# Kernel tuning notes

Measured on AMD Instinct MI355X. Metric: run time of the kernel, lower is better.

Reference implementation:

```python
import jax, jax.numpy as jnp
import numpy as np

B, H, S, D = 4, 16, 2048, 64


def setup_inputs() -> dict:
    key = jax.random.key(0)
    kq, kk, kv = jax.random.split(key, 3)
    Q = jax.random.normal(kq, (B, H, S, D), dtype=jnp.float32)
    K = jax.random.normal(kk, (B, H, S, D), dtype=jnp.float32)
    V = jax.random.normal(kv, (B, H, S, D), dtype=jnp.float32)
    mask = jnp.ones((1, 1, S, S), dtype=jnp.int32)
    return {"Q": Q, "K": K, "V": V, "mask": mask}


def reference(Q, K, V, mask):
    d_k = Q.shape[-1]
    scale = 1.0 / jnp.sqrt(jnp.asarray(d_k, dtype=Q.dtype))
    # [B, H, S, S] attention scores
    attn = jnp.einsum('bhqd,bhkd->bhqk', Q, K) * scale
    # mask == 0 -> -1e9 (matches torch boolean-index assignment)
    attn = jnp.where(mask == 0, jnp.asarray(-1e9, dtype=attn.dtype), attn)
    softmax_attn = jax.nn.softmax(attn, axis=-1)
    out = jnp.einsum('bhqk,bhkd->bhqd', softmax_attn, V)
    return out
```

## Files before the change

### kernel.cpp

```cpp
#include <hip/hip_runtime.h>

typedef __bf16 bf16;
typedef __attribute__((ext_vector_type(8))) __bf16 bf16x8;
typedef __attribute__((ext_vector_type(8))) ushort ushort8v;
typedef __attribute__((ext_vector_type(4))) ushort ushort4v;
typedef __attribute__((ext_vector_type(16))) float f32x16;

constexpr int S_LEN = 2048;
constexpr int DH    = 64;
constexpr int QBLK  = 128;
constexpr int KVBLK = 64;
constexpr int NWAVE = 4;
constexpr int NT    = S_LEN / KVBLK;
constexpr float QSCALE = 0.125f * 1.44269504088896f;
constexpr float NEG    = -1.44269504e9f;
constexpr float THR    = 8.0f;
constexpr size_t TILE_BYTES = (size_t)KVBLK * DH * 2;
constexpr size_t KV_BYTES   = (size_t)64 * NT * TILE_BYTES;

__device__ __forceinline__ ushort bfb(float f) {
  bf16 b = (bf16)f;
  return __builtin_bit_cast(ushort, b);
}
__device__ __forceinline__ int SWZ(int row) {
  return ((row & 7) ^ ((row >> 3) & 7)) << 4;
}
__device__ __forceinline__ uint cvtpk(float lo, float hi) {
  uint r;
  asm("v_cvt_pk_bf16_f32 %0, %1, %2" : "=v"(r) : "v"(lo), "v"(hi));
  return r;
}
__device__ __forceinline__ void gload16(const char* g, void* l) {
  __builtin_amdgcn_global_load_lds(
      (__attribute__((address_space(1))) void*)(g),
      (__attribute__((address_space(3))) void*)(l), 16, 0, 0);
}

__global__ __launch_bounds__(256)
void cvt_kv(const float* __restrict__ K, const float* __restrict__ V,
            const int* __restrict__ M, char* __restrict__ kws,
            char* __restrict__ vws, uint* __restrict__ F) {
  const int t = blockIdx.x, bh = blockIdx.y, tid = threadIdx.x;
  const float* Kb = K + ((size_t)bh * S_LEN + t * KVBLK) * DH;
  const float* Vb = V + ((size_t)bh * S_LEN + t * KVBLK) * DH;
  char* kd = kws + ((size_t)bh * NT + t) * TILE_BYTES;
  char* vd = vws + ((size_t)bh * NT + t) * TILE_BYTES;

  const int kr0 = tid >> 3, kc8 = tid & 7;
#pragma unroll
  for (int h = 0; h < 2; ++h) {
    const int row = kr0 + 32 * h;
    const float* kp = Kb + (size_t)row * DH + kc8 * 8;
    float4 a = *(const float4*)kp;
    float4 b = *(const float4*)(kp + 4);
    ushort8v pk;
    pk[0]=bfb(a.x); pk[1]=bfb(a.y); pk[2]=bfb(a.z); pk[3]=bfb(a.w);
    pk[4]=bfb(b.x); pk[5]=bfb(b.y); pk[6]=bfb(b.z); pk[7]=bfb(b.w);
    *(ushort8v*)(kd + row * 128 + ((kc8 * 16) ^ SWZ(row))) = pk;
  }
  const int vr = (tid >> 4) * 4, vc = (tid & 15) * 4;
  float rr[4][4];
#pragma unroll
  for (int i = 0; i < 4; ++i)
    *(float4*)rr[i] = *(const float4*)(Vb + (size_t)(vr + i) * DH + vc);
#pragma unroll
  for (int c = 0; c < 4; ++c) {
    const int d = vc + c;
    ushort4v p4;
    p4[0]=bfb(rr[0][c]); p4[1]=bfb(rr[1][c]);
    p4[2]=bfb(rr[2][c]); p4[3]=bfb(rr[3][c]);
    *(ushort4v*)(vd + d * 128 + ((vr * 2) ^ SWZ(d))) = p4;
  }

  if (bh < 8) {
    const int qt = t, g = bh;
    const int r  = tid >> 2;
    const int c0 = (tid & 3) * 16;
    __shared__ int s[4];
    uint bits = 0;
    for (int i = 0; i < 4; ++i) {
      const int kt = g * 4 + i;
      const int* row = M + (size_t)(qt * 64 + r) * S_LEN + kt * 64 + c0;
      int ok = 1;
#pragma unroll
      for (int j = 0; j < 4; ++j) {
        int4 v = *(const int4*)(row + j * 4);
        ok &= (v.x != 0) & (v.y != 0) & (v.z != 0) & (v.w != 0);
      }
      ok = __all(ok) ? 1 : 0;
      if ((tid & 63) == 0) s[tid >> 6] = ok;
      __syncthreads();
      if (s[0] & s[1] & s[2] & s[3]) bits |= 1u << kt;
      __syncthreads();
    }
    if (tid == 0) F[qt * 8 + g] = bits;
  }
}

template<bool PRE>
__global__ __launch_bounds__(256, 4)
void attn_fwd(const float* __restrict__ Q, const float* __restrict__ K,
              const float* __restrict__ V, const int* __restrict__ M,
              const uint* __restrict__ F, const char* __restrict__ kws,
              const char* __restrict__ vws, float* __restrict__ O)
{
  __shared__ __align__(16) ushort kb[KVBLK * DH];
  __shared__ __align__(16) ushort vb[KVBLK * DH];

  const int tid  = threadIdx.x;
  const int lane = tid & 63;
  const int w    = tid >> 6;
  const int ql   = lane & 31;
  const int h    = lane >> 5;

  const int flat = blockIdx.y * gridDim.x + blockIdx.x;
  const int nid  = (flat & 7) * 128 + (flat >> 3);
  const int q0   = (nid & 15) * QBLK;
  const int bh   = nid >> 4;

  const float* Qb = Q + ((size_t)bh * S_LEN) * DH;
  const float* Kb = K + ((size_t)bh * S_LEN) * DH;
  const float* Vb = V + ((size_t)bh * S_LEN) * DH;

  uint fmask = 0u;
  if (PRE) {
    uint fm0 = 0u, fm1 = 0u;
#pragma unroll
    for (int g = 0; g < 8; ++g) {
      fm0 |= F[(q0 >> 6) * 8 + g];
      fm1 |= F[((q0 >> 6) + 1) * 8 + g];
    }
    fmask = fm0 & fm1;
  }

  bf16x8 qf[4];
  {
    const float* qp = Qb + (size_t)(q0 + w * 32 + ql) * DH + 8 * h;
#pragma unroll
    for (int s = 0; s < 4; ++s) {
      float4 a = *(const float4*)(qp + 16 * s);
      float4 b = *(const float4*)(qp + 16 * s + 4);
      bf16x8 t2;
      t2[0]=(bf16)(a.x*QSCALE); t2[1]=(bf16)(a.y*QSCALE);
      t2[2]=(bf16)(a.z*QSCALE); t2[3]=(bf16)(a.w*QSCALE);
      t2[4]=(bf16)(b.x*QSCALE); t2[5]=(bf16)(b.y*QSCALE);
      t2[6]=(bf16)(b.z*QSCALE); t2[7]=(bf16)(b.w*QSCALE);
      qf[s] = t2;
    }
  }

  f32x16 acc0, acc1;
#pragma unroll
  for (int i = 0; i < 16; ++i) { acc0[i] = 0.f; acc1[i] = 0.f; }
  float mrow = -1e30f;
  float rsum = 0.f;

  int kofs[2][4];
#pragma unroll
  for (int x = 0; x < 2; ++x) {
    const int row = 32 * x + ql;
    const int sw  = SWZ(row);
#pragma unroll
    for (int s = 0; s < 4; ++s)
      kofs[x][s] = row * 128 + ((32 * s + 16 * h) ^ sw);
  }

  auto mkfrag = [&](float p0, float p1, float p2, float p3,
                    float p4, float p5, float p6, float p7) -> bf16x8 {
    uint a0 = cvtpk(p0, p1), a1 = cvtpk(p2, p3);
    uint b0 = cvtpk(p4, p5), b1 = cvtpk(p6, p7);
    uint ta0 = __shfl_xor(a0, 32), ta1 = __shfl_xor(a1, 32);
    uint tb0 = __shfl_xor(b0, 32), tb1 = __shfl_xor(b1, 32);
    uint4 wv;
    wv.x = h ? tb0 : a0;
    wv.y = h ? tb1 : a1;
    wv.z = h ? b0  : ta0;
    wv.w = h ? b1  : ta1;
    return __builtin_bit_cast(bf16x8, wv);
  };

  const int kr0 = tid >> 3, kc8 = tid & 7;
  const int vr = (tid >> 4) * 4, vc = (tid & 15) * 4;

  for (int t = 0; t < NT; ++t) {
    if (PRE) {
      const char* ksrc = kws + ((size_t)bh * NT + t) * TILE_BYTES;
      const char* vsrc = vws + ((size_t)bh * NT + t) * TILE_BYTES;
#pragma unroll
      for (int c = 0; c < 2; ++c) {
        const int off = (w + c * 4) * 1024 + lane * 16;
        gload16(ksrc + off, (char*)kb + off);
        gload16(vsrc + off, (char*)vb + off);
      }
    } else {
#pragma unroll
      for (int hh = 0; hh < 2; ++hh) {
        const int row = kr0 + 32 * hh;
        const float* kp = Kb + (size_t)(t * KVBLK + row) * DH + kc8 * 8;
        float4 a = *(const float4*)kp;
        float4 b = *(const float4*)(kp + 4);
        ushort8v pk;
        pk[0]=bfb(a.x); pk[1]=bfb(a.y); pk[2]=bfb(a.z); pk[3]=bfb(a.w);
        pk[4]=bfb(b.x); pk[5]=bfb(b.y); pk[6]=bfb(b.z); pk[7]=bfb(b.w);
        *(ushort8v*)((char*)kb + row * 128 + ((kc8 * 16) ^ SWZ(row))) = pk;
      }
      float rr[4][4];
#pragma unroll
      for (int i = 0; i < 4; ++i)
        *(float4*)rr[i] = *(const float4*)(Vb + (size_t)(t * KVBLK + vr + i) * DH + vc);
#pragma unroll
      for (int c = 0; c < 4; ++c) {
        const int d = vc + c;
        ushort4v p4;
        p4[0]=bfb(rr[0][c]); p4[1]=bfb(rr[1][c]);
        p4[2]=bfb(rr[2][c]); p4[3]=bfb(rr[3][c]);
        *(ushort4v*)((char*)vb + d * 128 + ((vr * 2) ^ SWZ(d))) = p4;
      }
    }
    __syncthreads();

    f32x16 sc0, sc1;
#pragma unroll
    for (int i = 0; i < 16; ++i) { sc0[i] = 0.f; sc1[i] = 0.f; }

    __builtin_amdgcn_s_setprio(1);
#pragma unroll
    for (int s = 0; s < 4; ++s) {
      bf16x8 k0 = *(const bf16x8*)((const char*)kb + kofs[0][s]);
      bf16x8 k1 = *(const bf16x8*)((const char*)kb + kofs[1][s]);
      sc0 = __builtin_amdgcn_mfma_f32_32x32x16_bf16(k0, qf[s], sc0, 0,0,0);
      sc1 = __builtin_amdgcn_mfma_f32_32x32x16_bf16(k1, qf[s], sc1, 0,0,0);
    }
    __builtin_amdgcn_s_setprio(0);

    const bool allset = PRE ? (((fmask >> t) & 1u) != 0u) : false;
    if (!allset) {
      const size_t mo = (size_t)(q0 + w * 32 + ql) * S_LEN + t * KVBLK + 4 * h;
#pragma unroll
      for (int r = 0; r < 16; ++r) {
        const int cr = (r & 3) + 8 * (r >> 2);
        if (M[mo + cr] == 0)      sc0[r] = NEG;
        if (M[mo + 32 + cr] == 0) sc1[r] = NEG;
      }
    }

    float lm = fmaxf(sc0[0], sc0[1]);
#pragma unroll
    for (int i = 2; i < 16; ++i) lm = fmaxf(lm, sc0[i]);
#pragma unroll
    for (int i = 0; i < 16; ++i) lm = fmaxf(lm, sc1[i]);
    lm = fmaxf(lm, __shfl_xor(lm, 32));

    if (!__all(lm - mrow <= THR)) {
      const float mnew = fmaxf(mrow, lm);
      const float corr = __builtin_amdgcn_exp2f(mrow - mnew);
      rsum *= corr;
      acc0 *= corr;
      acc1 *= corr;
      mrow = mnew;
    }

    float ps = 0.f;
#pragma unroll
    for (int i = 0; i < 16; ++i) {
      sc0[i] = __builtin_amdgcn_exp2f(sc0[i] - mrow); ps += sc0[i];
      sc1[i] = __builtin_amdgcn_exp2f(sc1[i] - mrow); ps += sc1[i];
    }
    rsum += ps;

    bf16x8 pf[4];
    pf[0] = mkfrag(sc0[0], sc0[1], sc0[2],  sc0[3],  sc0[4],  sc0[5],  sc0[6],  sc0[7]);
    pf[1] = mkfrag(sc0[8], sc0[9], sc0[10], sc0[11], sc0[12], sc0[13], sc0[14], sc0[15]);
    pf[2] = mkfrag(sc1[0], sc1[1], sc1[2],  sc1[3],  sc1[4],  sc1[5],  sc1[6],  sc1[7]);
    pf[3] = mkfrag(sc1[8], sc1[9], sc1[10], sc1[11], sc1[12], sc1[13], sc1[14], sc1[15]);

    __builtin_amdgcn_s_setprio(1);
#pragma unroll
    for (int s = 0; s < 4; ++s) {
      bf16x8 v0 = *(const bf16x8*)((const char*)vb + kofs[0][s]);
      bf16x8 v1 = *(const bf16x8*)((const char*)vb + kofs[1][s]);
      acc0 = __builtin_amdgcn_mfma_f32_32x32x16_bf16(v0, pf[s], acc0, 0,0,0);
      acc1 = __builtin_amdgcn_mfma_f32_32x32x16_bf16(v1, pf[s], acc1, 0,0,0);
    }
    __builtin_amdgcn_s_setprio(0);

    __syncthreads();
  }

  rsum += __shfl_xor(rsum, 32);
  const float inv = 1.0f / rsum;
  float* Ob = O + ((size_t)bh * S_LEN + q0 + w * 32 + ql) * DH + 4 * h;
#pragma unroll
  for (int g = 0; g < 4; ++g) {
    float4 o0 = { acc0[4*g+0]*inv, acc0[4*g+1]*inv, acc0[4*g+2]*inv, acc0[4*g+3]*inv };
    float4 o1 = { acc1[4*g+0]*inv, acc1[4*g+1]*inv, acc1[4*g+2]*inv, acc1[4*g+3]*inv };
    *(float4*)(Ob + 8 * g)      = o0;
    *(float4*)(Ob + 32 + 8 * g) = o1;
  }
}

extern "C" void kernel_launch(void* const* d_in, const int* in_sizes, int n_in,
                              void* d_out, int out_size, void* d_ws, size_t ws_size,
                              hipStream_t stream)
{
  const float* Q = (const float*)d_in[0];
  const float* K = (const float*)d_in[1];
  const float* V = (const float*)d_in[2];
  const int*   M = (const int*)d_in[3];
  float* O = (float*)d_out;

  const size_t need = 4096 + 2 * KV_BYTES;
  const bool pre = (d_ws != nullptr) && (ws_size >= need);

  dim3 grid(S_LEN / QBLK, 4 * 16);
  if (pre) {
    uint* F   = (uint*)d_ws;
    char* kws = (char*)d_ws + 4096;
    char* vws = kws + KV_BYTES;
    cvt_kv<<<dim3(NT, 64), 256, 0, stream>>>(K, V, M, kws, vws, F);
    attn_fwd<true><<<grid, NWAVE * 64, 0, stream>>>(Q, K, V, M, F, kws, vws, O);
  } else {
    attn_fwd<false><<<grid, NWAVE * 64, 0, stream>>>(Q, K, V, M, nullptr, nullptr, nullptr, O);
  }
}
```

Measured before the change: 114.7 us.

## Load two KV tiles per barrier pair in the prepacked attention path

In the prepacked path, each iteration now loads two consecutive 64-row K/V tiles into doubled LDS buffers and processes both before the closing barrier. This halves the number of barrier pairs and load rounds per block, cutting synchronisation stalls. In exchange LDS per block doubles and launch bounds drop from 4 to 3 blocks per CU, which lowers occupancy and reduces latency hiding. The compute body is moved into a shared lambda used by both paths.

```diff
diff --git a/kernel.cpp b/kernel.cpp
--- a/kernel.cpp
+++ b/kernel.cpp
@@ -12,6 +12,7 @@
 constexpr int KVBLK = 64;
 constexpr int NWAVE = 4;
 constexpr int NT    = S_LEN / KVBLK;
+constexpr int NT2   = NT / 2;
 constexpr float QSCALE = 0.125f * 1.44269504088896f;
 constexpr float NEG    = -1.44269504e9f;
 constexpr float THR    = 8.0f;
@@ -98,14 +99,14 @@
 }
 
 template<bool PRE>
-__global__ __launch_bounds__(256, 4)
+__global__ __launch_bounds__(256, 3)
 void attn_fwd(const float* __restrict__ Q, const float* __restrict__ K,
               const float* __restrict__ V, const int* __restrict__ M,
               const uint* __restrict__ F, const char* __restrict__ kws,
               const char* __restrict__ vws, float* __restrict__ O)
 {
-  __shared__ __align__(16) ushort kb[KVBLK * DH];
-  __shared__ __align__(16) ushort vb[KVBLK * DH];
+  __shared__ __align__(16) ushort kb[2 * KVBLK * DH];
+  __shared__ __align__(16) ushort vb[2 * KVBLK * DH];
 
   const int tid  = threadIdx.x;
   const int lane = tid & 63;
@@ -179,20 +180,93 @@
     return __builtin_bit_cast(bf16x8, wv);
   };
 
+  auto compute = [&](int t64, int base) {
+    f32x16 sc0, sc1;
+#pragma unroll
+    for (int i = 0; i < 16; ++i) { sc0[i] = 0.f; sc1[i] = 0.f; }
+
+    __builtin_amdgcn_s_setprio(1);
+#pragma unroll
+    for (int s = 0; s < 4; ++s) {
+      bf16x8 k0 = *(const bf16x8*)((const char*)kb + base + kofs[0][s]);
+      bf16x8 k1 = *(const bf16x8*)((const char*)kb + base + kofs[1][s]);
+      sc0 = __builtin_amdgcn_mfma_f32_32x32x16_bf16(k0, qf[s], sc0, 0,0,0);
+      sc1 = __builtin_amdgcn_mfma_f32_32x32x16_bf16(k1, qf[s], sc1, 0,0,0);
+    }
+    __builtin_amdgcn_s_setprio(0);
+
+    const bool allset = PRE ? (((fmask >> t64) & 1u) != 0u) : false;
+    if (!allset) {
+      const size_t mo = (size_t)(q0 + w * 32 + ql) * S_LEN + t64 * KVBLK + 4 * h;
+#pragma unroll
+      for (int r = 0; r < 16; ++r) {
+        const int cr = (r & 3) + 8 * (r >> 2);
+        if (M[mo + cr] == 0)      sc0[r] = NEG;
+        if (M[mo + 32 + cr] == 0) sc1[r] = NEG;
+      }
+    }
+
+    float lm = fmaxf(sc0[0], sc0[1]);
+#pragma unroll
+    for (int i = 2; i < 16; ++i) lm = fmaxf(lm, sc0[i]);
+#pragma unroll
+    for (int i = 0; i < 16; ++i) lm = fmaxf(lm, sc1[i]);
+    lm = fmaxf(lm, __shfl_xor(lm, 32));
+
+    if (!__all(lm - mrow <= THR)) {
+      const float mnew = fmaxf(mrow, lm);
+      const float corr = __builtin_amdgcn_exp2f(mrow - mnew);
+      rsum *= corr;
+      acc0 *= corr;
+      acc1 *= corr;
+      mrow = mnew;
+    }
+
+    float ps = 0.f;
+#pragma unroll
+    for (int i = 0; i < 16; ++i) {
+      sc0[i] = __builtin_amdgcn_exp2f(sc0[i] - mrow); ps += sc0[i];
+      sc1[i] = __builtin_amdgcn_exp2f(sc1[i] - mrow); ps += sc1[i];
+    }
+    rsum += ps;
+
+    bf16x8 pf[4];
+    pf[0] = mkfrag(sc0[0], sc0[1], sc0[2],  sc0[3],  sc0[4],  sc0[5],  sc0[6],  sc0[7]);
+    pf[1] = mkfrag(sc0[8], sc0[9], sc0[10], sc0[11], sc0[12], sc0[13], sc0[14], sc0[15]);
+    pf[2] = mkfrag(sc1[0], sc1[1], sc1[2],  sc1[3],  sc1[4],  sc1[5],  sc1[6],  sc1[7]);
+    pf[3] = mkfrag(sc1[8], sc1[9], sc1[10], sc1[11], sc1[12], sc1[13], sc1[14], sc1[15]);
+
+    __builtin_amdgcn_s_setprio(1);
+#pragma unroll
+    for (int s = 0; s < 4; ++s) {
+      bf16x8 v0 = *(const bf16x8*)((const char*)vb + base + kofs[0][s]);
+      bf16x8 v1 = *(const bf16x8*)((const char*)vb + base + kofs[1][s]);
+      acc0 = __builtin_amdgcn_mfma_f32_32x32x16_bf16(v0, pf[s], acc0, 0,0,0);
+      acc1 = __builtin_amdgcn_mfma_f32_32x32x16_bf16(v1, pf[s], acc1, 0,0,0);
+    }
+    __builtin_amdgcn_s_setprio(0);
+  };
+
   const int kr0 = tid >> 3, kc8 = tid & 7;
   const int vr = (tid >> 4) * 4, vc = (tid & 15) * 4;
 
-  for (int t = 0; t < NT; ++t) {
-    if (PRE) {
-      const char* ksrc = kws + ((size_t)bh * NT + t) * TILE_BYTES;
-      const char* vsrc = vws + ((size_t)bh * NT + t) * TILE_BYTES;
-#pragma unroll
-      for (int c = 0; c < 2; ++c) {
+  if constexpr (PRE) {
+    for (int tt = 0; tt < NT2; ++tt) {
+      const char* ksrc = kws + ((size_t)bh * NT + 2 * tt) * TILE_BYTES;
+      const char* vsrc = vws + ((size_t)bh * NT + 2 * tt) * TILE_BYTES;
+#pragma unroll
+      for (int c = 0; c < 4; ++c) {
         const int off = (w + c * 4) * 1024 + lane * 16;
         gload16(ksrc + off, (char*)kb + off);
         gload16(vsrc + off, (char*)vb + off);
       }
-    } else {
+      __syncthreads();
+      compute(2 * tt,     0);
+      compute(2 * tt + 1, 8192);
+      __syncthreads();
+    }
+  } else {
+    for (int t = 0; t < NT; ++t) {
 #pragma unroll
       for (int hh = 0; hh < 2; ++hh) {
         const int row = kr0 + 32 * hh;
@@ -216,75 +290,10 @@
         p4[2]=bfb(rr[2][c]); p4[3]=bfb(rr[3][c]);
         *(ushort4v*)((char*)vb + d * 128 + ((vr * 2) ^ SWZ(d))) = p4;
       }
-    }
-    __syncthreads();
-
-    f32x16 sc0, sc1;
-#pragma unroll
-    for (int i = 0; i < 16; ++i) { sc0[i] = 0.f; sc1[i] = 0.f; }
-
-    __builtin_amdgcn_s_setprio(1);
-#pragma unroll
-    for (int s = 0; s < 4; ++s) {
-      bf16x8 k0 = *(const bf16x8*)((const char*)kb + kofs[0][s]);
-      bf16x8 k1 = *(const bf16x8*)((const char*)kb + kofs[1][s]);
-      sc0 = __builtin_amdgcn_mfma_f32_32x32x16_bf16(k0, qf[s], sc0, 0,0,0);
-      sc1 = __builtin_amdgcn_mfma_f32_32x32x16_bf16(k1, qf[s], sc1, 0,0,0);
-    }
-    __builtin_amdgcn_s_setprio(0);
-
-    const bool allset = PRE ? (((fmask >> t) & 1u) != 0u) : false;
-    if (!allset) {
-      const size_t mo = (size_t)(q0 + w * 32 + ql) * S_LEN + t * KVBLK + 4 * h;
-#pragma unroll
-      for (int r = 0; r < 16; ++r) {
-        const int cr = (r & 3) + 8 * (r >> 2);
-        if (M[mo + cr] == 0)      sc0[r] = NEG;
-        if (M[mo + 32 + cr] == 0) sc1[r] = NEG;
-      }
-    }
-
-    float lm = fmaxf(sc0[0], sc0[1]);
-#pragma unroll
-    for (int i = 2; i < 16; ++i) lm = fmaxf(lm, sc0[i]);
-#pragma unroll
-    for (int i = 0; i < 16; ++i) lm = fmaxf(lm, sc1[i]);
-    lm = fmaxf(lm, __shfl_xor(lm, 32));
-
-    if (!__all(lm - mrow <= THR)) {
-      const float mnew = fmaxf(mrow, lm);
-      const float corr = __builtin_amdgcn_exp2f(mrow - mnew);
-      rsum *= corr;
-      acc0 *= corr;
-      acc1 *= corr;
-      mrow = mnew;
-    }
-
-    float ps = 0.f;
-#pragma unroll
-    for (int i = 0; i < 16; ++i) {
-      sc0[i] = __builtin_amdgcn_exp2f(sc0[i] - mrow); ps += sc0[i];
-      sc1[i] = __builtin_amdgcn_exp2f(sc1[i] - mrow); ps += sc1[i];
-    }
-    rsum += ps;
-
-    bf16x8 pf[4];
-    pf[0] = mkfrag(sc0[0], sc0[1], sc0[2],  sc0[3],  sc0[4],  sc0[5],  sc0[6],  sc0[7]);
-    pf[1] = mkfrag(sc0[8], sc0[9], sc0[10], sc0[11], sc0[12], sc0[13], sc0[14], sc0[15]);
-    pf[2] = mkfrag(sc1[0], sc1[1], sc1[2],  sc1[3],  sc1[4],  sc1[5],  sc1[6],  sc1[7]);
-    pf[3] = mkfrag(sc1[8], sc1[9], sc1[10], sc1[11], sc1[12], sc1[13], sc1[14], sc1[15]);
-
-    __builtin_amdgcn_s_setprio(1);
-#pragma unroll
-    for (int s = 0; s < 4; ++s) {
-      bf16x8 v0 = *(const bf16x8*)((const char*)vb + kofs[0][s]);
-      bf16x8 v1 = *(const bf16x8*)((const char*)vb + kofs[1][s]);
-      acc0 = __builtin_amdgcn_mfma_f32_32x32x16_bf16(v0, pf[s], acc0, 0,0,0);
-      acc1 = __builtin_amdgcn_mfma_f32_32x32x16_bf16(v1, pf[s], acc1, 0,0,0);
-    }
-    __builtin_amdgcn_s_setprio(0);
-
-    __syncthreads();
+      __syncthreads();
+      compute(t, 0);
+      __syncthreads();
+    }
   }
 
   rsum += __shfl_xor(rsum, 32);
```

After: 120.6 us. +5.2%, slower.
